# Kernel tuning notes

Measured on AMD Instinct MI355X. Metric: run time of the kernel, lower is better.

The kernel has to match this reference:

```python
import jax, jax.numpy as jnp
import numpy as np

N = 50000      # nodes
E = 800000     # edges (avg degree 16)
G = 50         # graphs in batch (1000 nodes each)
D_IN, H, H2, OUT = 8, 128, 64, 1


def setup_inputs() -> dict:
    key = jax.random.key(0)
    ks = jax.random.split(key, 16)
    src = jax.random.randint(ks[0], (E,), 0, N)
    # every node gets at least one in-edge (forward computes 3/in_deg)
    dst = jnp.concatenate([jnp.arange(N), jax.random.randint(ks[1], (E - N,), 0, N)])
    graph_ids = jnp.arange(N) // (N // G)

    def lin(k, fan_in, fan_out):
        return jax.random.normal(k, (fan_in, fan_out), jnp.float32) / np.float32(np.sqrt(fan_in))

    inp = {"src": src, "dst": dst, "graph_ids": graph_ids}
    dims = [(D_IN, H), (H, H), (H, H), (H, H), (H, H)]
    for i, (fi, fo) in enumerate(dims):
        inp[f"W{i+1}"] = lin(ks[2 + i], fi, fo)
        inp[f"b{i+1}"] = jnp.zeros((fo,), jnp.float32)
    inp["lw1"] = lin(ks[8], H, H2)
    inp["lb1"] = jnp.zeros((H2,), jnp.float32)
    inp["lw2"] = lin(ks[9], H2, OUT)
    inp["lb2"] = jnp.zeros((OUT,), jnp.float32)
    return inp


def reference(src, dst, graph_ids, W1, b1, W2, b2, W3, b3, W4, b4, W5, b5, lw1, lb1, lw2, lb2):
    ones_e = jnp.ones((E,), jnp.float32)
    in_deg = jax.ops.segment_sum(ones_e, dst, num_segments=N)   # [N]
    out_deg = jax.ops.segment_sum(ones_e, src, num_segments=N)  # [N]

    # degree features (8 channels)
    h1 = in_deg[:, None]
    h2 = (in_deg > 3.0).astype(jnp.float32)[:, None]
    h3 = 3.0 / h1
    h4 = (in_deg > 4.0).astype(jnp.float32)[:, None]
    h_ = jnp.concatenate([h1, h2, h3, h4, -h1, -h2, -h3, -h4], axis=1)  # [N,8]

    # DGL GraphConv norm='both': clamp degrees to min 1 for normalization
    norm_src = jnp.maximum(out_deg, 1.0) ** -0.5  # [N]
    norm_dst = jnp.maximum(in_deg, 1.0) ** -0.5   # [N]

    def conv(h, W, b):
        m = (h * norm_src[:, None])[src]                        # [E, d] gather
        agg = jax.ops.segment_sum(m, dst, num_segments=N)       # [N, d] scatter-add
        return agg * norm_dst[:, None] @ W + b

    h_co = jax.nn.relu(conv(h_, W1, b1))
    h_co = jax.nn.relu(conv(h_co, W2, b2))
    h_co = jax.nn.relu(conv(h_co, W3, b3))
    h_co = jax.nn.relu(conv(h_co, W4, b4))
    h_co = jax.nn.relu(conv(h_co, W5, b5))                      # [N, H]

    # dgl.mean_nodes: per-graph mean pool
    counts = jax.ops.segment_sum(jnp.ones((N,), jnp.float32), graph_ids, num_segments=G)
    graph_emb = jax.ops.segment_sum(h_co, graph_ids, num_segments=G) / counts[:, None]  # [G, H]

    # dropout layers are identity in eval mode
    h_emb = jax.nn.relu(graph_emb @ lw1 + lb1)
    pred = jax.nn.sigmoid(h_emb @ lw2 + lb2)                    # [G, 1]
    return (pred, graph_emb, h_co)
```

## Files before the change

kernel.cpp:

```cpp
#include <hip/hip_runtime.h>
#include <math.h>

#define N_NODES 50000
#define N_EDGES 800000
#define N_GRAPHS 50
#define HD 128
#define TM 64
#define LDA 68
#define POOL_CHUNK 125
#define SCAN_B 256
#define SCAN_NB ((N_NODES + SCAN_B - 1) / SCAN_B)

__global__ void k_degrees(const int* __restrict__ src, const int* __restrict__ dst,
                          int* deg_in, int* deg_out) {
    int e = blockIdx.x * blockDim.x + threadIdx.x;
    if (e < N_EDGES) {
        atomicAdd(&deg_in[dst[e]], 1);
        atomicAdd(&deg_out[src[e]], 1);
    }
}

__global__ void k_norms(const int* __restrict__ deg_in, const int* __restrict__ deg_out,
                        const int* __restrict__ gids,
                        float* norm_src, float* norm_dst, int* gcount,
                        float4* __restrict__ feat4) {
    __shared__ int hist[N_GRAPHS];
    int t = threadIdx.x;
    if (t < N_GRAPHS) hist[t] = 0;
    __syncthreads();
    int i = blockIdx.x * blockDim.x + t;
    if (i < N_NODES) {
        float di = (float)deg_in[i];
        float dq = (float)deg_out[i];
        float nd = 1.0f / sqrtf(fmaxf(di, 1.0f));
        float ns = 1.0f / sqrtf(fmaxf(dq, 1.0f));
        norm_dst[i] = nd;
        norm_src[i] = ns;
        float4 f;
        f.x = di * ns;
        f.y = (di > 3.0f) ? ns : 0.0f;
        f.z = (3.0f / di) * ns;
        f.w = (di > 4.0f) ? ns : 0.0f;
        feat4[i] = f;
        atomicAdd(&hist[gids[i]], 1);
    }
    __syncthreads();
    if (t < N_GRAPHS && hist[t] != 0) atomicAdd(&gcount[t], hist[t]);
}

__global__ void k_scan1(const int* __restrict__ deg_in, int* off, int* bsum) {
    __shared__ int sh[SCAN_B];
    int t = threadIdx.x;
    int i = blockIdx.x * SCAN_B + t;
    int v = (i < N_NODES) ? deg_in[i] : 0;
    sh[t] = v;
    __syncthreads();
    for (int o = 1; o < SCAN_B; o <<= 1) {
        int u = (t >= o) ? sh[t - o] : 0;
        __syncthreads();
        sh[t] += u;
        __syncthreads();
    }
    if (i < N_NODES) off[i] = sh[t] - v;
    if (t == SCAN_B - 1) bsum[blockIdx.x] = sh[t];
}

__global__ void k_scan2(int* bsum, int* off) {
    __shared__ int sh[SCAN_B];
    int t = threadIdx.x;
    int v = (t < SCAN_NB) ? bsum[t] : 0;
    sh[t] = v;
    __syncthreads();
    for (int o = 1; o < SCAN_B; o <<= 1) {
        int u = (t >= o) ? sh[t - o] : 0;
        __syncthreads();
        sh[t] += u;
        __syncthreads();
    }
    if (t < SCAN_NB) bsum[t] = sh[t] - v;
    if (t == SCAN_B - 1) off[N_NODES] = sh[t];
}

__global__ void k_scan3(int* off, const int* __restrict__ bsum, int* cursor) {
    int b = blockIdx.x, t = threadIdx.x;
    int i = b * SCAN_B + t;
    if (i < N_NODES) {
        int o = off[i] + bsum[b];
        off[i] = o;
        cursor[i] = o;
    }
}

__global__ void k_scatter(const int* __restrict__ src, const int* __restrict__ dst,
                          int* cursor, int* csr) {
    int e = blockIdx.x * blockDim.x + threadIdx.x;
    if (e < N_EDGES) {
        int p = atomicAdd(&cursor[dst[e]], 1);
        csr[p] = src[e];
    }
}

__global__ void k_agg1(const int* __restrict__ off, const int* __restrict__ csr,
                       const float4* __restrict__ feat4,
                       const float* __restrict__ ndst, float* __restrict__ agg8) {
    int i = blockIdx.x * blockDim.x + threadIdx.x;
    if (i >= N_NODES) return;
    int e0 = off[i], e1 = off[i + 1];
    float a0 = 0.f, a1 = 0.f, a2 = 0.f, a3 = 0.f;
    int e = e0;
    for (; e + 1 < e1; e += 2) {
        float4 f0 = feat4[csr[e]];
        float4 f1 = feat4[csr[e + 1]];
        a0 += f0.x + f1.x; a1 += f0.y + f1.y;
        a2 += f0.z + f1.z; a3 += f0.w + f1.w;
    }
    if (e < e1) {
        float4 f0 = feat4[csr[e]];
        a0 += f0.x; a1 += f0.y; a2 += f0.z; a3 += f0.w;
    }
    float nd = ndst[i];
    a0 *= nd; a1 *= nd; a2 *= nd; a3 *= nd;
    float4* p = (float4*)(agg8 + (size_t)i * 8);
    float4 hi = { a0, a1, a2, a3 };
    float4 lo = { -a0, -a1, -a2, -a3 };
    p[0] = hi;
    p[1] = lo;
}

__global__ void k_gemm1(const float* __restrict__ agg8, const float* __restrict__ W,
                        const float* __restrict__ b, const float* __restrict__ nsrc,
                        float* __restrict__ out) {
    __shared__ float Wsh[8 * 128];
    int t = threadIdx.x;
    for (int i = t; i < 1024; i += 256) Wsh[i] = W[i];
    __syncthreads();
    int row = blockIdx.x * 2 + (t >> 7);
    int j = t & 127;
    if (row >= N_NODES) return;
    const float* a = agg8 + (size_t)row * 8;
    float acc = b[j];
#pragma unroll
    for (int k = 0; k < 8; ++k) acc += a[k] * Wsh[k * 128 + j];
    out[(size_t)row * HD + j] = fmaxf(acc, 0.0f) * nsrc[row];
}

__global__ void k_agg4(const int* __restrict__ off, const int* __restrict__ csr,
                       const float* __restrict__ ndst,
                       const float* __restrict__ h, float* __restrict__ out) {
    int wid = (blockIdx.x * blockDim.x + threadIdx.x) >> 6;
    int lane = threadIdx.x & 63;
    if (wid >= N_NODES) return;
    int half = lane >> 5;
    int q = lane & 31;
    int e0 = off[wid], e1 = off[wid + 1];
    float4 a = { 0.f, 0.f, 0.f, 0.f };
    int e = e0 + half;
    for (; e + 2 < e1; e += 4) {
        int s0 = csr[e], s1 = csr[e + 2];
        float4 v0 = *(const float4*)(h + (size_t)s0 * HD + q * 4);
        float4 v1 = *(const float4*)(h + (size_t)s1 * HD + q * 4);
        a.x += v0.x + v1.x; a.y += v0.y + v1.y;
        a.z += v0.z + v1.z; a.w += v0.w + v1.w;
    }
    if (e < e1) {
        int s0 = csr[e];
        float4 v0 = *(const float4*)(h + (size_t)s0 * HD + q * 4);
        a.x += v0.x; a.y += v0.y; a.z += v0.z; a.w += v0.w;
    }
    a.x += __shfl_xor(a.x, 32);
    a.y += __shfl_xor(a.y, 32);
    a.z += __shfl_xor(a.z, 32);
    a.w += __shfl_xor(a.w, 32);
    if (half == 0) {
        float nd = ndst[wid];
        a.x *= nd; a.y *= nd; a.z *= nd; a.w *= nd;
        *(float4*)(out + (size_t)wid * HD + q * 4) = a;
    }
}

__global__ void k_agg2(const int* __restrict__ off, const int* __restrict__ csr,
                       const float* __restrict__ ndst,
                       const float* __restrict__ h, float* __restrict__ out) {
    int wid = (blockIdx.x * blockDim.x + threadIdx.x) >> 6;
    int lane = threadIdx.x & 63;
    if (wid >= N_NODES) return;
    int e0 = off[wid], e1 = off[wid + 1];
    float a0 = 0.f, a1 = 0.f;
    int e = e0;
    for (; e + 3 < e1; e += 4) {
        int s0 = csr[e], s1 = csr[e + 1], s2 = csr[e + 2], s3 = csr[e + 3];
        float2 v0 = *(const float2*)(h + (size_t)s0 * HD + lane * 2);
        float2 v1 = *(const float2*)(h + (size_t)s1 * HD + lane * 2);
        float2 v2 = *(const float2*)(h + (size_t)s2 * HD + lane * 2);
        float2 v3 = *(const float2*)(h + (size_t)s3 * HD + lane * 2);
        a0 += v0.x + v1.x + v2.x + v3.x;
        a1 += v0.y + v1.y + v2.y + v3.y;
    }
    for (; e < e1; ++e) {
        int s0 = csr[e];
        float2 v0 = *(const float2*)(h + (size_t)s0 * HD + lane * 2);
        a0 += v0.x; a1 += v0.y;
    }
    float nd = ndst[wid];
    float2 o; o.x = a0 * nd; o.y = a1 * nd;
    *(float2*)(out + (size_t)wid * HD + lane * 2) = o;
}

__global__ __launch_bounds__(512) void k_gemm(const float* __restrict__ A,
                                              const float* __restrict__ W,
                                              const float* __restrict__ b,
                                              const float* __restrict__ nsrc,
                                              int premult,
                                              float* __restrict__ out) {
    __shared__ float Wsh[128 * 128];
    __shared__ float Ash[128 * LDA];
    int t = threadIdx.x;
    const float4* W4 = (const float4*)W;
    float4* Wsh4 = (float4*)Wsh;
#pragma unroll
    for (int i = 0; i < 8; ++i) Wsh4[t + i * 512] = W4[t + i * 512];
    int row0 = blockIdx.x * TM;
#pragma unroll
    for (int i = 0; i < 4; ++i) {
        int idx = t + i * 512;
        int r = idx >> 5;
        int q = idx & 31;
        int row = row0 + r;
        if (row >= N_NODES) row = N_NODES - 1;
        float4 v = ((const float4*)(A + (size_t)row * HD))[q];
        Ash[(4 * q + 0) * LDA + r] = v.x;
        Ash[(4 * q + 1) * LDA + r] = v.y;
        Ash[(4 * q + 2) * LDA + r] = v.z;
        Ash[(4 * q + 3) * LDA + r] = v.w;
    }
    __syncthreads();
    int j0 = (t & 31) * 4;
    int r0 = (t >> 5) * 4;
    float4 bv = *(const float4*)(b + j0);
    float acc[4][4];
#pragma unroll
    for (int r = 0; r < 4; ++r) {
        acc[r][0] = bv.x; acc[r][1] = bv.y; acc[r][2] = bv.z; acc[r][3] = bv.w;
    }
#pragma unroll 4
    for (int k = 0; k < 128; ++k) {
        float4 w = *(const float4*)&Wsh[k * 128 + j0];
        float4 a = *(const float4*)&Ash[k * LDA + r0];
        acc[0][0] += a.x * w.x; acc[0][1] += a.x * w.y; acc[0][2] += a.x * w.z; acc[0][3] += a.x * w.w;
        acc[1][0] += a.y * w.x; acc[1][1] += a.y * w.y; acc[1][2] += a.y * w.z; acc[1][3] += a.y * w.w;
        acc[2][0] += a.z * w.x; acc[2][1] += a.z * w.y; acc[2][2] += a.z * w.z; acc[2][3] += a.z * w.w;
        acc[3][0] += a.w * w.x; acc[3][1] += a.w * w.y; acc[3][2] += a.w * w.z; acc[3][3] += a.w * w.w;
    }
#pragma unroll
    for (int r = 0; r < 4; ++r) {
        int row = row0 + r0 + r;
        if (row < N_NODES) {
            float sc = premult ? nsrc[row] : 1.0f;
            float* op = out + (size_t)row * HD + j0;
            float2 o01 = { fmaxf(acc[r][0], 0.f) * sc, fmaxf(acc[r][1], 0.f) * sc };
            float2 o23 = { fmaxf(acc[r][2], 0.f) * sc, fmaxf(acc[r][3], 0.f) * sc };
            *(float2*)op = o01;
            *(float2*)(op + 2) = o23;
        }
    }
}

__global__ void k_pool(const float* __restrict__ hco, const int* __restrict__ gids,
                       float* gsum) {
    int f = threadIdx.x;
    int n0 = blockIdx.x * POOL_CHUNK;
    int g = gids[n0];
    float s = 0.f;
    for (int i = 0; i < POOL_CHUNK; ++i)
        s += hco[(size_t)(n0 + i) * HD + f];
    atomicAdd(&gsum[g * HD + f], s);
}

__global__ void k_head(const float* __restrict__ gsum, const int* __restrict__ gcount,
                       const float* __restrict__ lw1, const float* __restrict__ lb1,
                       const float* __restrict__ lw2, const float* __restrict__ lb2,
                       float* __restrict__ dout) {
    __shared__ float ge[128];
    int g = blockIdx.x, j = threadIdx.x;
    float cnt = (float)gcount[g];
    float g0 = gsum[g * HD + j] / cnt;
    float g1 = gsum[g * HD + 64 + j] / cnt;
    ge[j] = g0; ge[64 + j] = g1;
    dout[N_GRAPHS + g * HD + j] = g0;
    dout[N_GRAPHS + g * HD + 64 + j] = g1;
    __syncthreads();
    float acc = lb1[j];
#pragma unroll 4
    for (int k = 0; k < 128; ++k) acc += ge[k] * lw1[k * 64 + j];
    float he = fmaxf(acc, 0.f);
    float p = he * lw2[j];
#pragma unroll
    for (int o = 32; o > 0; o >>= 1) p += __shfl_down(p, o);
    if (j == 0) dout[g] = 1.0f / (1.0f + expf(-(p + lb2[0])));
}

extern "C" void kernel_launch(void* const* d_in, const int* in_sizes, int n_in,
                              void* d_out, int out_size, void* d_ws, size_t ws_size,
                              hipStream_t stream) {
    const int* src  = (const int*)d_in[0];
    const int* dst  = (const int*)d_in[1];
    const int* gids = (const int*)d_in[2];
    const float* W1 = (const float*)d_in[3];  const float* b1 = (const float*)d_in[4];
    const float* W2 = (const float*)d_in[5];  const float* b2 = (const float*)d_in[6];
    const float* W3 = (const float*)d_in[7];  const float* b3 = (const float*)d_in[8];
    const float* W4 = (const float*)d_in[9];  const float* b4 = (const float*)d_in[10];
    const float* W5 = (const float*)d_in[11]; const float* b5 = (const float*)d_in[12];
    const float* lw1 = (const float*)d_in[13]; const float* lb1 = (const float*)d_in[14];
    const float* lw2 = (const float*)d_in[15]; const float* lb2 = (const float*)d_in[16];
    float* out = (float*)d_out;

    char* ws = (char*)d_ws;
    int*    deg_in   = (int*)(ws + 0);
    int*    deg_out  = (int*)(ws + 200192);
    int*    gcount   = (int*)(ws + 400384);
    float*  gsum     = (float*)(ws + 400640);
    const size_t ZERO_BYTES = 426240;
    int*    off      = (int*)(ws + 426240);
    int*    cursor   = (int*)(ws + 626432);
    int*    csr      = (int*)(ws + 826624);
    float*  norm_src = (float*)(ws + 4026624);
    float*  norm_dst = (float*)(ws + 4226816);
    int*    bsum     = (int*)(ws + 4427008);
    float4* feat4    = (float4*)(ws + 4428032);
    float*  aggbuf   = (float*)(ws + 5228288);
    float*  hws      = (float*)(ws + 30828288);
    const size_t WS_NEEDED = 30828288 + 25600000;

    float* hco = out + (N_GRAPHS + N_GRAPHS * HD);
    bool aligned = (ws_size >= WS_NEEDED);
    float* hbuf = aligned ? hws : hco;

    hipMemsetAsync(ws, 0, ZERO_BYTES, stream);

    k_degrees<<<(N_EDGES + 255) / 256, 256, 0, stream>>>(src, dst, deg_in, deg_out);
    k_norms<<<(N_NODES + 255) / 256, 256, 0, stream>>>(deg_in, deg_out, gids,
                                                       norm_src, norm_dst, gcount, feat4);
    k_scan1<<<SCAN_NB, SCAN_B, 0, stream>>>(deg_in, off, bsum);
    k_scan2<<<1, SCAN_B, 0, stream>>>(bsum, off);
    k_scan3<<<SCAN_NB, SCAN_B, 0, stream>>>(off, bsum, cursor);
    k_scatter<<<(N_EDGES + 255) / 256, 256, 0, stream>>>(src, dst, cursor, csr);

    k_agg1<<<(N_NODES + 255) / 256, 256, 0, stream>>>(off, csr, feat4, norm_dst, aggbuf);
    k_gemm1<<<N_NODES / 2, 256, 0, stream>>>(aggbuf, W1, b1, norm_src, hbuf);

    const float* Ws[4] = { W2, W3, W4, W5 };
    const float* bs[4] = { b2, b3, b4, b5 };
    for (int L = 0; L < 4; ++L) {
        if (aligned)
            k_agg4<<<(N_NODES * 64 + 255) / 256, 256, 0, stream>>>(off, csr,
                                                                   norm_dst, hbuf, aggbuf);
        else
            k_agg2<<<(N_NODES * 64 + 255) / 256, 256, 0, stream>>>(off, csr,
                                                                   norm_dst, hbuf, aggbuf);
        float* gout = (L < 3) ? hbuf : hco;
        k_gemm<<<(N_NODES + TM - 1) / TM, 512, 0, stream>>>(aggbuf, Ws[L], bs[L],
                                                            norm_src, (L < 3) ? 1 : 0,
                                                            gout);
    }

    k_pool<<<N_NODES / POOL_CHUNK, 128, 0, stream>>>(hco, gids, gsum);
    k_head<<<N_GRAPHS, 64, 0, stream>>>(gsum, gcount, lw1, lb1, lw2, lb2, out);
}
```

Before: 576.4 us.

## Replace global atomic degree counting with per-block LDS histograms and reduction

Degree counting now builds per-block shared-memory histograms with two nodes packed into each 32-bit counter, writes the partial histograms to the aggregation buffer, and sums them in a separate reduction kernel. This removes contended global atomics and shrinks the zeroing memset, because the degree arrays no longer need clearing. In exchange it writes and reads about 25 MB of partial histograms, adds an extra launch, and runs only 128 large-LDS blocks.

```diff
diff --git a/kernel.cpp b/kernel.cpp
--- a/kernel.cpp
+++ b/kernel.cpp
@@ -10,14 +10,51 @@
 #define POOL_CHUNK 125
 #define SCAN_B 256
 #define SCAN_NB ((N_NODES + SCAN_B - 1) / SCAN_B)
-
-__global__ void k_degrees(const int* __restrict__ src, const int* __restrict__ dst,
-                          int* deg_in, int* deg_out) {
-    int e = blockIdx.x * blockDim.x + threadIdx.x;
-    if (e < N_EDGES) {
-        atomicAdd(&deg_in[dst[e]], 1);
-        atomicAdd(&deg_out[src[e]], 1);
-    }
+#define NB_H 128
+#define CH_H (N_EDGES / NB_H)
+#define NBIN2 (N_NODES / 2)
+
+__global__ __launch_bounds__(256) void k_hist(const int* __restrict__ src,
+                                              const int* __restrict__ dst,
+                                              unsigned* __restrict__ part_in,
+                                              unsigned* __restrict__ part_out) {
+    __shared__ unsigned cnt[NBIN2];
+    int t = threadIdx.x, b = blockIdx.x;
+    int e0 = b * CH_H;
+    for (int j = t; j < NBIN2; j += 256) cnt[j] = 0;
+    __syncthreads();
+    for (int e = e0 + t; e < e0 + CH_H; e += 256) {
+        int i = dst[e];
+        atomicAdd(&cnt[i >> 1], 1u << ((i & 1) * 16));
+    }
+    __syncthreads();
+    for (int j = t; j < NBIN2; j += 256) part_in[b * NBIN2 + j] = cnt[j];
+    __syncthreads();
+    for (int j = t; j < NBIN2; j += 256) cnt[j] = 0;
+    __syncthreads();
+    for (int e = e0 + t; e < e0 + CH_H; e += 256) {
+        int i = src[e];
+        atomicAdd(&cnt[i >> 1], 1u << ((i & 1) * 16));
+    }
+    __syncthreads();
+    for (int j = t; j < NBIN2; j += 256) part_out[b * NBIN2 + j] = cnt[j];
+}
+
+__global__ void k_dreduce(const unsigned* __restrict__ part_in,
+                          const unsigned* __restrict__ part_out,
+                          int* __restrict__ deg_in, int* __restrict__ deg_out) {
+    int j = blockIdx.x * blockDim.x + threadIdx.x;
+    if (j >= NBIN2) return;
+    unsigned ilo = 0, ihi = 0, olo = 0, ohi = 0;
+#pragma unroll 4
+    for (int b = 0; b < NB_H; ++b) {
+        unsigned pi = part_in[b * NBIN2 + j];
+        unsigned po = part_out[b * NBIN2 + j];
+        ilo += pi & 0xFFFFu; ihi += pi >> 16;
+        olo += po & 0xFFFFu; ohi += po >> 16;
+    }
+    ((int2*)deg_in)[j] = make_int2((int)ilo, (int)ihi);
+    ((int2*)deg_out)[j] = make_int2((int)olo, (int)ohi);
 }
 
 __global__ void k_norms(const int* __restrict__ deg_in, const int* __restrict__ deg_out,
@@ -315,21 +352,24 @@
     float* out = (float*)d_out;
 
     char* ws = (char*)d_ws;
-    int*    deg_in   = (int*)(ws + 0);
-    int*    deg_out  = (int*)(ws + 200192);
-    int*    gcount   = (int*)(ws + 400384);
-    float*  gsum     = (float*)(ws + 400640);
-    const size_t ZERO_BYTES = 426240;
-    int*    off      = (int*)(ws + 426240);
-    int*    cursor   = (int*)(ws + 626432);
-    int*    csr      = (int*)(ws + 826624);
-    float*  norm_src = (float*)(ws + 4026624);
-    float*  norm_dst = (float*)(ws + 4226816);
-    int*    bsum     = (int*)(ws + 4427008);
-    float4* feat4    = (float4*)(ws + 4428032);
-    float*  aggbuf   = (float*)(ws + 5228288);
-    float*  hws      = (float*)(ws + 30828288);
-    const size_t WS_NEEDED = 30828288 + 25600000;
+    int*    gcount   = (int*)(ws + 0);
+    float*  gsum     = (float*)(ws + 256);
+    const size_t ZERO_BYTES = 25856;
+    int*    deg_in   = (int*)(ws + 26112);
+    int*    deg_out  = (int*)(ws + 226304);
+    int*    off      = (int*)(ws + 426496);
+    int*    cursor   = (int*)(ws + 626688);
+    int*    csr      = (int*)(ws + 826880);
+    float*  norm_src = (float*)(ws + 4026880);
+    float*  norm_dst = (float*)(ws + 4227072);
+    int*    bsum     = (int*)(ws + 4427264);
+    float4* feat4    = (float4*)(ws + 4428288);
+    float*  aggbuf   = (float*)(ws + 5228544);
+    float*  hws      = (float*)(ws + 30828544);
+    const size_t WS_NEEDED = 30828544 + 25600000;
+
+    unsigned* part_in  = (unsigned*)aggbuf;
+    unsigned* part_out = (unsigned*)aggbuf + NB_H * NBIN2;
 
     float* hco = out + (N_GRAPHS + N_GRAPHS * HD);
     bool aligned = (ws_size >= WS_NEEDED);
@@ -337,7 +377,9 @@
 
     hipMemsetAsync(ws, 0, ZERO_BYTES, stream);
 
-    k_degrees<<<(N_EDGES + 255) / 256, 256, 0, stream>>>(src, dst, deg_in, deg_out);
+    k_hist<<<NB_H, 256, 0, stream>>>(src, dst, part_in, part_out);
+    k_dreduce<<<(NBIN2 + 255) / 256, 256, 0, stream>>>(part_in, part_out,
+                                                       deg_in, deg_out);
     k_norms<<<(N_NODES + 255) / 256, 256, 0, stream>>>(deg_in, deg_out, gids,
                                                        norm_src, norm_dst, gcount, feat4);
     k_scan1<<<SCAN_NB, SCAN_B, 0, stream>>>(deg_in, off, bsum);
```

Measured after the change: 540.5 us. -6.2%, faster.
